# Optimization experiments

Measured on AMD Instinct MI355X. Metric: run time of the kernel, lower is better.

## Reference

```python
import jax, jax.numpy as jnp
import numpy as np

NUM_SEGMENTS = 4096  # number of graphs in the batch
E = 2097152          # number of edges
IN_CH = 64
HID_CH = 2 * IN_CH


def setup_inputs() -> dict:
    key = jax.random.key(0)
    k1, k2, k3, k4 = jax.random.split(key, 4)
    edge_attr = jax.random.normal(k1, (E, IN_CH), dtype=jnp.float32)
    batch = jnp.sort(jax.random.randint(k2, (E,), 0, NUM_SEGMENTS, dtype=jnp.int32))
    # MLP params: Linear(in, 2*in) -> ReLU -> Linear(2*in, 1)
    s1 = 1.0 / np.sqrt(IN_CH)
    s2 = 1.0 / np.sqrt(HID_CH)
    w1 = jax.random.uniform(k3, (IN_CH, HID_CH), jnp.float32, -s1, s1)
    b1 = jnp.zeros((HID_CH,), jnp.float32)
    w2 = jax.random.uniform(k4, (HID_CH, 1), jnp.float32, -s2, s2)
    b2 = jnp.zeros((1,), jnp.float32)
    return {"edge_attr": edge_attr, "w1": w1, "b1": b1, "w2": w2, "b2": b2, "batch": batch}


def reference(edge_attr, w1, b1, w2, b2, batch):
    # Tiny MLP scorer: [E, C] -> [E]
    h = jax.nn.relu(edge_attr @ w1 + b1)           # [E, 2C]
    score = (h @ w2 + b2).reshape(-1)              # [E]
    # Segment (per-graph) softmax keyed by `batch`, as in torch_geometric.utils.softmax
    seg_max = jax.ops.segment_max(score, batch, num_segments=NUM_SEGMENTS)  # [G]
    seg_max = jnp.where(jnp.isfinite(seg_max), seg_max, 0.0)  # empty segments
    ex = jnp.exp(score - seg_max[batch])           # [E]
    denom = jax.ops.segment_sum(ex, batch, num_segments=NUM_SEGMENTS)       # [G]
    return ex / (denom[batch] + 1e-16)
```

## Files before the change

### kernel.cpp

```cpp
#include <hip/hip_runtime.h>
#include <hip/hip_bf16.h>
#include <math.h>

typedef _Float16 half8  __attribute__((ext_vector_type(8)));
typedef __fp16   fp16x2 __attribute__((ext_vector_type(2)));
typedef float    floatx4 __attribute__((ext_vector_type(4)));

#define IN_CH 64
#define HID   128
#define NSEG  4096

__device__ __forceinline__ unsigned fkey(float s) {
    unsigned u = __float_as_uint(s);
    return (u & 0x80000000u) ? ~u : (u | 0x80000000u);
}
__device__ __forceinline__ float funkey(unsigned k) {
    unsigned u = (k & 0x80000000u) ? (k ^ 0x80000000u) : ~k;
    return __uint_as_float(u);
}

__global__ void init_seg(unsigned* __restrict__ segkey, float* __restrict__ denom) {
    int i = blockIdx.x * blockDim.x + threadIdx.x;
    if (i < NSEG) { segkey[i] = 0u; denom[i] = 0.0f; }
}

__global__ __launch_bounds__(256, 2) void mlp_score(
    const float* __restrict__ x, const float* __restrict__ w1,
    const float* __restrict__ b1, const float* __restrict__ w2,
    const float* __restrict__ b2, float* __restrict__ score, int E)
{
    const int tid  = threadIdx.x;
    const int lane = tid & 63;
    const int wid  = tid >> 6;
    const int g    = lane >> 4;
    const int l15  = lane & 15;

    half8 afr[2][8];
#pragma unroll
    for (int ks = 0; ks < 2; ++ks)
#pragma unroll
        for (int ct = 0; ct < 8; ++ct) {
            const float* wp = w1 + (size_t)(ks * 32 + g * 8) * HID + ct * 16 + l15;
            half8 h;
#pragma unroll
            for (int j = 0; j < 8; ++j) h[j] = (_Float16)wp[(size_t)j * HID];
            afr[ks][ct] = h;
        }

    floatx4 biasC[8], w2r[8];
#pragma unroll
    for (int ct = 0; ct < 8; ++ct)
#pragma unroll
        for (int r = 0; r < 4; ++r) {
            biasC[ct][r] = b1[ct * 16 + g * 4 + r];
            w2r[ct][r]   = w2[ct * 16 + g * 4 + r];
        }
    const float b2v = b2[0];

    const int nwtile = E >> 4;
    const int wstep  = (int)gridDim.x * 4;
    const size_t laneoff = (size_t)l15 * IN_CH + g * 8;

#define LOADSET(F, T) do {                                            \
        const float* xr = x + (size_t)(T) * (16 * IN_CH) + laneoff;   \
        F##0 = *(const floatx4*)(xr);                                 \
        F##1 = *(const floatx4*)(xr + 4);                             \
        F##2 = *(const floatx4*)(xr + 32);                            \
        F##3 = *(const floatx4*)(xr + 36);                            \
    } while (0)

    union H8 { half8 h8; fp16x2 h2[4]; };

#define COMPUTE(F, T) do {                                            \
        H8 ub, uc;                                                    \
        ub.h2[0] = __builtin_amdgcn_cvt_pkrtz(F##0[0], F##0[1]);      \
        ub.h2[1] = __builtin_amdgcn_cvt_pkrtz(F##0[2], F##0[3]);      \
        ub.h2[2] = __builtin_amdgcn_cvt_pkrtz(F##1[0], F##1[1]);      \
        ub.h2[3] = __builtin_amdgcn_cvt_pkrtz(F##1[2], F##1[3]);      \
        uc.h2[0] = __builtin_amdgcn_cvt_pkrtz(F##2[0], F##2[1]);      \
        uc.h2[1] = __builtin_amdgcn_cvt_pkrtz(F##2[2], F##2[3]);      \
        uc.h2[2] = __builtin_amdgcn_cvt_pkrtz(F##3[0], F##3[1]);      \
        uc.h2[3] = __builtin_amdgcn_cvt_pkrtz(F##3[2], F##3[3]);      \
        floatx4 acc[8];                                               \
        _Pragma("unroll")                                             \
        for (int ct = 0; ct < 8; ++ct)                                \
            acc[ct] = __builtin_amdgcn_mfma_f32_16x16x32_f16(afr[0][ct], ub.h8, biasC[ct], 0, 0, 0); \
        _Pragma("unroll")                                             \
        for (int ct = 0; ct < 8; ++ct)                                \
            acc[ct] = __builtin_amdgcn_mfma_f32_16x16x32_f16(afr[1][ct], uc.h8, acc[ct], 0, 0, 0);   \
        float s0 = 0.f, s1 = 0.f, s2 = 0.f, s3 = 0.f;                 \
        _Pragma("unroll")                                             \
        for (int ct = 0; ct < 8; ++ct) {                              \
            s0 += fmaxf(acc[ct][0], 0.f) * w2r[ct][0];                \
            s1 += fmaxf(acc[ct][1], 0.f) * w2r[ct][1];                \
            s2 += fmaxf(acc[ct][2], 0.f) * w2r[ct][2];                \
            s3 += fmaxf(acc[ct][3], 0.f) * w2r[ct][3];                \
        }                                                             \
        float s = (s0 + s1) + (s2 + s3);                              \
        s += __shfl_xor(s, 16);                                       \
        s += __shfl_xor(s, 32);                                       \
        if (lane < 16)                                                \
            score[(T) * 16 + l15] = s + b2v;                          \
    } while (0)

    int wt = blockIdx.x * 4 + wid;
    if (wt < nwtile) {
        floatx4 fA0, fA1, fA2, fA3, fB0, fB1, fB2, fB3;
        LOADSET(fA, wt);
        for (;;) {
            int nxt = wt + wstep;
            bool hn = (nxt < nwtile);
            if (hn) LOADSET(fB, nxt);
            COMPUTE(fA, wt);
            if (!hn) break;
            wt = nxt;
            nxt = wt + wstep;
            hn = (nxt < nwtile);
            if (hn) LOADSET(fA, nxt);
            COMPUTE(fB, wt);
            if (!hn) break;
            wt = nxt;
        }
    }
#undef LOADSET
#undef COMPUTE
}

__global__ __launch_bounds__(256) void seg_max(
    const float* __restrict__ score, const int* __restrict__ batch,
    unsigned* __restrict__ segkey, int E)
{
    int t = blockIdx.x * 256 + threadIdx.x;
    int i0 = t * 8;
    if (i0 + 8 > E) return;
    int4 bA = *(const int4*)(batch + i0);
    int4 bB = *(const int4*)(batch + i0 + 4);
    floatx4 sA = *(const floatx4*)(score + i0);
    floatx4 sB = *(const floatx4*)(score + i0 + 4);
    int   ids[8] = {bA.x, bA.y, bA.z, bA.w, bB.x, bB.y, bB.z, bB.w};
    float ss[8]  = {sA[0], sA[1], sA[2], sA[3], sB[0], sB[1], sB[2], sB[3]};
    int cur = ids[0];
    float m = ss[0];
#pragma unroll
    for (int j = 1; j < 8; ++j) {
        if (ids[j] == cur) {
            m = fmaxf(m, ss[j]);
        } else {
            atomicMax(segkey + cur, fkey(m));
            cur = ids[j];
            m = ss[j];
        }
    }
    atomicMax(segkey + cur, fkey(m));
}

__global__ __launch_bounds__(256) void seg_denom(
    const float* __restrict__ score, const int* __restrict__ batch,
    const unsigned* __restrict__ segkey, float* __restrict__ denom, int E)
{
    int t = blockIdx.x * 256 + threadIdx.x;
    int i0 = t * 8;
    if (i0 + 8 > E) return;
    int4 bA = *(const int4*)(batch + i0);
    int4 bB = *(const int4*)(batch + i0 + 4);
    floatx4 sA = *(const floatx4*)(score + i0);
    floatx4 sB = *(const floatx4*)(score + i0 + 4);
    int   ids[8] = {bA.x, bA.y, bA.z, bA.w, bB.x, bB.y, bB.z, bB.w};
    float ss[8]  = {sA[0], sA[1], sA[2], sA[3], sB[0], sB[1], sB[2], sB[3]};
    int cur = ids[0];
    float m = funkey(segkey[cur]);
    float a = __expf(ss[0] - m);
#pragma unroll
    for (int j = 1; j < 8; ++j) {
        if (ids[j] == cur) {
            a += __expf(ss[j] - m);
        } else {
            atomicAdd(denom + cur, a);
            cur = ids[j];
            m = funkey(segkey[cur]);
            a = __expf(ss[j] - m);
        }
    }
    atomicAdd(denom + cur, a);
}

__global__ __launch_bounds__(256) void finalize(
    float* __restrict__ score, const int* __restrict__ batch,
    const unsigned* __restrict__ segkey, const float* __restrict__ denom, int E)
{
    int t = blockIdx.x * 256 + threadIdx.x;
    int i0 = t * 8;
    if (i0 + 8 > E) return;
    int4 bA = *(const int4*)(batch + i0);
    int4 bB = *(const int4*)(batch + i0 + 4);
    floatx4 sA = *(const floatx4*)(score + i0);
    floatx4 sB = *(const floatx4*)(score + i0 + 4);
    int   ids[8] = {bA.x, bA.y, bA.z, bA.w, bB.x, bB.y, bB.z, bB.w};
    float ss[8]  = {sA[0], sA[1], sA[2], sA[3], sB[0], sB[1], sB[2], sB[3]};
    floatx4 oA, oB;
#pragma unroll
    for (int j = 0; j < 4; ++j) {
        float mj = funkey(segkey[ids[j]]);
        oA[j] = __expf(ss[j] - mj) / (denom[ids[j]] + 1e-16f);
    }
#pragma unroll
    for (int j = 0; j < 4; ++j) {
        float mj = funkey(segkey[ids[j + 4]]);
        oB[j] = __expf(ss[j + 4] - mj) / (denom[ids[j + 4]] + 1e-16f);
    }
    *(floatx4*)(score + i0)     = oA;
    *(floatx4*)(score + i0 + 4) = oB;
}

extern "C" void kernel_launch(void* const* d_in, const int* in_sizes, int n_in,
                              void* d_out, int out_size, void* d_ws, size_t ws_size,
                              hipStream_t stream) {
    const float* x   = (const float*)d_in[0];
    const float* w1  = (const float*)d_in[1];
    const float* b1  = (const float*)d_in[2];
    const float* w2  = (const float*)d_in[3];
    const float* b2  = (const float*)d_in[4];
    const int* batch = (const int*)d_in[5];
    float* out = (float*)d_out;
    const int E = in_sizes[5];

    unsigned* segkey = (unsigned*)d_ws;
    float*    denom  = (float*)((char*)d_ws + NSEG * sizeof(unsigned));

    init_seg<<<(NSEG + 255) / 256, 256, 0, stream>>>(segkey, denom);
    mlp_score<<<1024, 256, 0, stream>>>(x, w1, b1, w2, b2, out, E);
    const int nthr = E / 8;
    seg_max   <<<nthr / 256, 256, 0, stream>>>(out, batch, segkey, E);
    seg_denom <<<nthr / 256, 256, 0, stream>>>(out, batch, segkey, denom, E);
    finalize  <<<nthr / 256, 256, 0, stream>>>(out, batch, segkey, denom, E);
}
```

Baseline: 191.5 us.

## Stream MLP input through LDS with 4-deep async global_load_lds pipeline

Replaces the register double-buffered input loads in mlp_score with a per-wave 4-stage ring in shared memory, filled by global_load_lds and gated by explicit vmcnt waits. This keeps three tiles of loads in flight per wave to hide HBM latency on the 512 MB input stream. The grid is halved to 512 blocks so each wave handles more tiles. It adds 64 KB of LDS per block, which limits occupancy, and relies on hand-placed waitcnt counts and sched barriers being correct.

Result: no change. 195.1 us (+1.9%).

```diff
diff --git a/kernel.cpp b/kernel.cpp
--- a/kernel.cpp
+++ b/kernel.cpp
@@ -29,6 +29,8 @@
     const float* __restrict__ b1, const float* __restrict__ w2,
     const float* __restrict__ b2, float* __restrict__ score, int E)
 {
+    __shared__ __align__(16) char smem[4 * 4 * 4 * 1024];
+
     const int tid  = threadIdx.x;
     const int lane = tid & 63;
     const int wid  = tid >> 6;
@@ -58,72 +60,108 @@
     const float b2v = b2[0];
 
     const int nwtile = E >> 4;
-    const int wstep  = (int)gridDim.x * 4;
+    const int TOTW   = (int)gridDim.x * 4;
+    const int gw     = blockIdx.x * 4 + wid;
+    const int n      = nwtile / TOTW;
+    const int rem    = nwtile - n * TOTW;
+
+    char* lwave = smem + wid * 16384;
     const size_t laneoff = (size_t)l15 * IN_CH + g * 8;
 
-#define LOADSET(F, T) do {                                            \
-        const float* xr = x + (size_t)(T) * (16 * IN_CH) + laneoff;   \
-        F##0 = *(const floatx4*)(xr);                                 \
-        F##1 = *(const floatx4*)(xr + 4);                             \
-        F##2 = *(const floatx4*)(xr + 32);                            \
-        F##3 = *(const floatx4*)(xr + 36);                            \
+    union H8 { half8 h8; fp16x2 h2[4]; };
+
+#define STAGE(I) do {                                                          \
+        int wt_ = gw + (I) * TOTW;                                             \
+        const float* gs = x + (size_t)wt_ * (16 * IN_CH) + laneoff;            \
+        char* lb = lwave + ((I) & 3) * 4096;                                   \
+        __builtin_amdgcn_global_load_lds((const __attribute__((address_space(1))) void*)(gs),      (__attribute__((address_space(3))) void*)(lb),        16, 0, 0); \
+        __builtin_amdgcn_global_load_lds((const __attribute__((address_space(1))) void*)(gs + 4),  (__attribute__((address_space(3))) void*)(lb + 1024), 16, 0, 0); \
+        __builtin_amdgcn_global_load_lds((const __attribute__((address_space(1))) void*)(gs + 32), (__attribute__((address_space(3))) void*)(lb + 2048), 16, 0, 0); \
+        __builtin_amdgcn_global_load_lds((const __attribute__((address_space(1))) void*)(gs + 36), (__attribute__((address_space(3))) void*)(lb + 3072), 16, 0, 0); \
     } while (0)
 
-    union H8 { half8 h8; fp16x2 h2[4]; };
-
-#define COMPUTE(F, T) do {                                            \
-        H8 ub, uc;                                                    \
-        ub.h2[0] = __builtin_amdgcn_cvt_pkrtz(F##0[0], F##0[1]);      \
-        ub.h2[1] = __builtin_amdgcn_cvt_pkrtz(F##0[2], F##0[3]);      \
-        ub.h2[2] = __builtin_amdgcn_cvt_pkrtz(F##1[0], F##1[1]);      \
-        ub.h2[3] = __builtin_amdgcn_cvt_pkrtz(F##1[2], F##1[3]);      \
-        uc.h2[0] = __builtin_amdgcn_cvt_pkrtz(F##2[0], F##2[1]);      \
-        uc.h2[1] = __builtin_amdgcn_cvt_pkrtz(F##2[2], F##2[3]);      \
-        uc.h2[2] = __builtin_amdgcn_cvt_pkrtz(F##3[0], F##3[1]);      \
-        uc.h2[3] = __builtin_amdgcn_cvt_pkrtz(F##3[2], F##3[3]);      \
-        floatx4 acc[8];                                               \
-        _Pragma("unroll")                                             \
-        for (int ct = 0; ct < 8; ++ct)                                \
+#define CORE(F0, F1, F2, F3, WT) do {                                          \
+        H8 ub, uc;                                                             \
+        ub.h2[0] = __builtin_amdgcn_cvt_pkrtz(F0[0], F0[1]);                   \
+        ub.h2[1] = __builtin_amdgcn_cvt_pkrtz(F0[2], F0[3]);                   \
+        ub.h2[2] = __builtin_amdgcn_cvt_pkrtz(F1[0], F1[1]);                   \
+        ub.h2[3] = __builtin_amdgcn_cvt_pkrtz(F1[2], F1[3]);                   \
+        uc.h2[0] = __builtin_amdgcn_cvt_pkrtz(F2[0], F2[1]);                   \
+        uc.h2[1] = __builtin_amdgcn_cvt_pkrtz(F2[2], F2[3]);                   \
+        uc.h2[2] = __builtin_amdgcn_cvt_pkrtz(F3[0], F3[1]);                   \
+        uc.h2[3] = __builtin_amdgcn_cvt_pkrtz(F3[2], F3[3]);                   \
+        floatx4 acc[8];                                                        \
+        _Pragma("unroll")                                                      \
+        for (int ct = 0; ct < 8; ++ct)                                         \
             acc[ct] = __builtin_amdgcn_mfma_f32_16x16x32_f16(afr[0][ct], ub.h8, biasC[ct], 0, 0, 0); \
-        _Pragma("unroll")                                             \
-        for (int ct = 0; ct < 8; ++ct)                                \
+        _Pragma("unroll")                                                      \
+        for (int ct = 0; ct < 8; ++ct)                                         \
             acc[ct] = __builtin_amdgcn_mfma_f32_16x16x32_f16(afr[1][ct], uc.h8, acc[ct], 0, 0, 0);   \
-        float s0 = 0.f, s1 = 0.f, s2 = 0.f, s3 = 0.f;                 \
-        _Pragma("unroll")                                             \
-        for (int ct = 0; ct < 8; ++ct) {                              \
-            s0 += fmaxf(acc[ct][0], 0.f) * w2r[ct][0];                \
-            s1 += fmaxf(acc[ct][1], 0.f) * w2r[ct][1];                \
-            s2 += fmaxf(acc[ct][2], 0.f) * w2r[ct][2];                \
-            s3 += fmaxf(acc[ct][3], 0.f) * w2r[ct][3];                \
-        }                                                             \
-        float s = (s0 + s1) + (s2 + s3);                              \
-        s += __shfl_xor(s, 16);                                       \
-        s += __shfl_xor(s, 32);                                       \
-        if (lane < 16)                                                \
-            score[(T) * 16 + l15] = s + b2v;                          \
+        float s0 = 0.f, s1 = 0.f, s2 = 0.f, s3 = 0.f;                          \
+        _Pragma("unroll")                                                      \
+        for (int ct = 0; ct < 8; ++ct) {                                       \
+            s0 += fmaxf(acc[ct][0], 0.f) * w2r[ct][0];                         \
+            s1 += fmaxf(acc[ct][1], 0.f) * w2r[ct][1];                         \
+            s2 += fmaxf(acc[ct][2], 0.f) * w2r[ct][2];                         \
+            s3 += fmaxf(acc[ct][3], 0.f) * w2r[ct][3];                         \
+        }                                                                      \
+        float s = (s0 + s1) + (s2 + s3);                                       \
+        s += __shfl_xor(s, 16);                                                \
+        s += __shfl_xor(s, 32);                                                \
+        if (lane < 16)                                                         \
+            score[(size_t)(WT) * 16 + l15] = s + b2v;                          \
     } while (0)
 
-    int wt = blockIdx.x * 4 + wid;
-    if (wt < nwtile) {
-        floatx4 fA0, fA1, fA2, fA3, fB0, fB1, fB2, fB3;
-        LOADSET(fA, wt);
-        for (;;) {
-            int nxt = wt + wstep;
-            bool hn = (nxt < nwtile);
-            if (hn) LOADSET(fB, nxt);
-            COMPUTE(fA, wt);
-            if (!hn) break;
-            wt = nxt;
-            nxt = wt + wstep;
-            hn = (nxt < nwtile);
-            if (hn) LOADSET(fA, nxt);
-            COMPUTE(fB, wt);
-            if (!hn) break;
-            wt = nxt;
-        }
-    }
-#undef LOADSET
-#undef COMPUTE
+#define BODY(I) do {                                                           \
+        const char* lb = lwave + ((I) & 3) * 4096 + lane * 16;                 \
+        floatx4 f0 = *(const floatx4*)(lb);                                    \
+        floatx4 f1 = *(const floatx4*)(lb + 1024);                             \
+        floatx4 f2 = *(const floatx4*)(lb + 2048);                             \
+        floatx4 f3 = *(const floatx4*)(lb + 3072);                             \
+        CORE(f0, f1, f2, f3, gw + (I) * TOTW);                                 \
+        __builtin_amdgcn_sched_barrier(0);                                     \
+    } while (0)
+
+    if (n >= 4) {
+        STAGE(0); STAGE(1); STAGE(2);
+        int i = 0;
+        for (; i < n - 3; ++i) {
+            STAGE(i + 3);
+            asm volatile("s_waitcnt vmcnt(12)" ::: "memory");
+            __builtin_amdgcn_sched_barrier(0);
+            BODY(i);
+        }
+        asm volatile("s_waitcnt vmcnt(8)" ::: "memory");
+        __builtin_amdgcn_sched_barrier(0);
+        BODY(i); ++i;
+        asm volatile("s_waitcnt vmcnt(4)" ::: "memory");
+        __builtin_amdgcn_sched_barrier(0);
+        BODY(i); ++i;
+        asm volatile("s_waitcnt vmcnt(0)" ::: "memory");
+        __builtin_amdgcn_sched_barrier(0);
+        BODY(i);
+    } else {
+        for (int i = 0; i < n; ++i) {
+            const float* xr = x + (size_t)(gw + i * TOTW) * (16 * IN_CH) + laneoff;
+            floatx4 f0 = *(const floatx4*)(xr);
+            floatx4 f1 = *(const floatx4*)(xr + 4);
+            floatx4 f2 = *(const floatx4*)(xr + 32);
+            floatx4 f3 = *(const floatx4*)(xr + 36);
+            CORE(f0, f1, f2, f3, gw + i * TOTW);
+        }
+    }
+    if (gw < rem) {
+        int wt_ = n * TOTW + gw;
+        const float* xr = x + (size_t)wt_ * (16 * IN_CH) + laneoff;
+        floatx4 f0 = *(const floatx4*)(xr);
+        floatx4 f1 = *(const floatx4*)(xr + 4);
+        floatx4 f2 = *(const floatx4*)(xr + 32);
+        floatx4 f3 = *(const floatx4*)(xr + 36);
+        CORE(f0, f1, f2, f3, wt_);
+    }
+#undef STAGE
+#undef CORE
+#undef BODY
 }
 
 __global__ __launch_bounds__(256) void seg_max(
@@ -228,7 +266,7 @@
     float*    denom  = (float*)((char*)d_ws + NSEG * sizeof(unsigned));
 
     init_seg<<<(NSEG + 255) / 256, 256, 0, stream>>>(segkey, denom);
-    mlp_score<<<1024, 256, 0, stream>>>(x, w1, b1, w2, b2, out, E);
+    mlp_score<<<512, 256, 0, stream>>>(x, w1, b1, w2, b2, out, E);
     const int nthr = E / 8;
     seg_max   <<<nthr / 256, 256, 0, stream>>>(out, batch, segkey, E);
     seg_denom <<<nthr / 256, 256, 0, stream>>>(out, batch, segkey, denom, E);
```
